# Kernel tuning notes

Measured on AMD Instinct MI355X. Metric: run time of the kernel, lower is better.

Reference implementation:

```python
import jax, jax.numpy as jnp
import numpy as np

B, S, D, UNITS = 32, 2048, 1024, 1024


def setup_inputs() -> dict:
    key = jax.random.key(0)
    ks = jax.random.split(key, 8)
    scale_d = 1.0 / np.sqrt(D)
    scale_u = 1.0 / np.sqrt(UNITS)
    return {
        "query": jax.random.normal(ks[0], (B, D), jnp.float32),
        "values": jax.random.normal(ks[1], (B, S, D), jnp.float32),
        "W1": jax.random.normal(ks[2], (D, UNITS), jnp.float32) * scale_d,
        "b1": jnp.zeros((UNITS,), jnp.float32),
        "W2": jax.random.normal(ks[3], (D, UNITS), jnp.float32) * scale_d,
        "b2": jnp.zeros((UNITS,), jnp.float32),
        "V": jax.random.normal(ks[4], (UNITS, 1), jnp.float32) * scale_u,
        "bV": jnp.zeros((1,), jnp.float32),
    }


def reference(query, values, W1, b1, W2, b2, V, bV):
    # proj of encoder outputs: [B, S, UNITS]
    proj_v = jnp.einsum("bsd,du->bsu", values, W1) + b1
    # proj of query (hidden), broadcast over sequence: [B, 1, UNITS]
    proj_q = (query @ W2 + b2)[:, None, :]
    # scalar score per position: [B, S, 1]
    score = jnp.tanh(proj_v + proj_q) @ V + bV
    # softmax over the sequence axis (axis=1)
    attention_weights = jax.nn.softmax(score, axis=1)  # [B, S, 1]
    # weighted sum of values: [B, D]
    context_vector = jnp.sum(attention_weights * values, axis=1)
    return context_vector, attention_weights
```

## Files before the change

### kernel.cpp

```cpp
#include <hip/hip_runtime.h>
#include <stdint.h>

typedef float f32x4 __attribute__((ext_vector_type(4)));
typedef short bf16x8 __attribute__((ext_vector_type(8)));

#define AS1 __attribute__((address_space(1)))
#define AS3 __attribute__((address_space(3)))

#define NB 32
#define NS 2048
#define ND 1024
#define NU 1024
#define NM (NB * NS)

__device__ __forceinline__ void glds16(const void* g, void* l) {
  __builtin_amdgcn_global_load_lds((const AS1 uint32_t*)g, (AS3 uint32_t*)l, 16, 0, 0);
}

__device__ __forceinline__ unsigned short bf16_rne(float f) {
  uint32_t u = __float_as_uint(f);
  u += 0x7fffu + ((u >> 16) & 1u);
  return (unsigned short)(u >> 16);
}

__device__ __forceinline__ uint32_t pack_bf16_trunc(float lo, float hi) {
  return __builtin_amdgcn_perm(__float_as_uint(hi), __float_as_uint(lo), 0x07060302u);
}

__device__ __forceinline__ float fast_tanh(float x) {
  float e = __expf(2.0f * x);
  return 1.0f - 2.0f / (e + 1.0f);
}

__global__ __launch_bounds__(256) void k_w1t(const float* __restrict__ W1,
                                             unsigned short* __restrict__ W1T) {
  __shared__ float t[64][65];
  const int n0 = blockIdx.x * 64, k0 = blockIdx.y * 64;
  const int tid = threadIdx.x;
  {
    const int r = tid >> 4, c4 = (tid & 15) << 2;
#pragma unroll
    for (int i = 0; i < 4; ++i) {
      f32x4 v = *(const f32x4*)(W1 + (size_t)(k0 + r + i * 16) * NU + n0 + c4);
      t[r + i * 16][c4 + 0] = v.x;
      t[r + i * 16][c4 + 1] = v.y;
      t[r + i * 16][c4 + 2] = v.z;
      t[r + i * 16][c4 + 3] = v.w;
    }
  }
  __syncthreads();
  const int rr = tid >> 2, cc = tid & 3;
  uint32_t o[8];
#pragma unroll
  for (int p = 0; p < 8; ++p) {
    float f0 = t[cc * 16 + 2 * p + 0][rr];
    float f1 = t[cc * 16 + 2 * p + 1][rr];
    o[p] = (uint32_t)bf16_rne(f0) | ((uint32_t)bf16_rne(f1) << 16);
  }
  unsigned short* dst = W1T + (size_t)(n0 + rr) * ND + k0 + cc * 16;
  *(uint4*)(dst + 0) = make_uint4(o[0], o[1], o[2], o[3]);
  *(uint4*)(dst + 8) = make_uint4(o[4], o[5], o[6], o[7]);
}

__global__ __launch_bounds__(256) void k_pq(const float* __restrict__ query,
                                            const float* __restrict__ W2,
                                            const float* __restrict__ b1,
                                            const float* __restrict__ b2,
                                            float* __restrict__ pq) {
  const int u = blockIdx.x * 256 + threadIdx.x;
  const int b = blockIdx.y;
  const float* q = query + b * ND;
  float a0 = b1[u] + b2[u], a1 = 0.f, a2 = 0.f, a3 = 0.f;
  for (int k = 0; k < ND; k += 16) {
#pragma unroll
    for (int j = 0; j < 16; j += 4) {
      a0 = fmaf(q[k + j + 0], W2[(size_t)(k + j + 0) * NU + u], a0);
      a1 = fmaf(q[k + j + 1], W2[(size_t)(k + j + 1) * NU + u], a1);
      a2 = fmaf(q[k + j + 2], W2[(size_t)(k + j + 2) * NU + u], a2);
      a3 = fmaf(q[k + j + 3], W2[(size_t)(k + j + 3) * NU + u], a3);
    }
  }
  pq[b * NU + u] = (a0 + a1) + (a2 + a3);
}

__global__ __launch_bounds__(256) void k_score(const float* __restrict__ values,
                                               const unsigned short* __restrict__ W1T,
                                               const float* __restrict__ pq,
                                               const float* __restrict__ V,
                                               float* __restrict__ score) {
  __shared__ f32x4 lds4[1536];
  char* lds = (char*)lds4;

  const int tid = threadIdx.x;
  const int lane = tid & 63;
  const int w = tid >> 6;
  const int wr = w >> 1, wc = w & 1;
  const int quad = lane >> 4, l15 = lane & 15;

  const int bid = blockIdx.x;
  const int xcd = bid & 7;
  const int local = bid >> 3;
  const int mt = xcd * 64 + (local >> 3);
  const int nc = local & 7;
  const int m0 = mt * 128, n0 = nc * 128;

  const char* aG[4];
  uint32_t aL[4];
  {
    const int p = lane & 7, r3 = lane >> 3;
    const int ca = p ^ r3;
#pragma unroll
    for (int i = 0; i < 4; ++i) {
      const int seg = w * 4 + i;
      const int mloc = seg * 8 + r3;
      aG[i] = (const char*)values + (size_t)(m0 + mloc) * (ND * 4) + ca * 16;
      aL[i] = seg * 1024;
    }
  }
  const char* bG[2];
  uint32_t bL[2];
  {
    const int cb = (lane & 3) ^ ((lane >> 3) & 3);
#pragma unroll
    for (int i = 0; i < 2; ++i) {
      const int seg = w * 2 + i;
      const int nloc = seg * 16 + (lane >> 2);
      bG[i] = (const char*)W1T + (size_t)(n0 + nloc) * (ND * 2) + cb * 16;
      bL[i] = 16384 + seg * 1024;
    }
  }

  uint32_t aOff[4][2], bOff[4];
  {
    const int p0 = (2 * quad) ^ (l15 & 7);
#pragma unroll
    for (int ri = 0; ri < 4; ++ri) {
      const int m = wr * 64 + ri * 16 + l15;
      aOff[ri][0] = m * 128 + p0 * 16;
      aOff[ri][1] = m * 128 + (p0 ^ 1) * 16;
    }
    const int pb = quad ^ ((l15 >> 1) & 3);
#pragma unroll
    for (int ci = 0; ci < 4; ++ci) {
      const int n = wc * 64 + ci * 16 + l15;
      bOff[ci] = 16384 + n * 64 + pb * 16;
    }
  }

  f32x4 acc[4][4];
#pragma unroll
  for (int i = 0; i < 4; ++i)
#pragma unroll
    for (int j = 0; j < 4; ++j) acc[i][j] = (f32x4){0.f, 0.f, 0.f, 0.f};

  for (int kt = 0; kt < 32; ++kt) {
    __syncthreads();
    const size_t aCol = (size_t)kt * 128;
    const size_t bCol = (size_t)kt * 64;
#pragma unroll
    for (int i = 0; i < 4; ++i) glds16(aG[i] + aCol, lds + aL[i]);
#pragma unroll
    for (int i = 0; i < 2; ++i) glds16(bG[i] + bCol, lds + bL[i]);
    __syncthreads();

    bf16x8 af[4];
#pragma unroll
    for (int ri = 0; ri < 4; ++ri) {
      f32x4 v0 = *(const f32x4*)(lds + aOff[ri][0]);
      f32x4 v1 = *(const f32x4*)(lds + aOff[ri][1]);
      union { uint32_t u[4]; bf16x8 v; } cvt;
      cvt.u[0] = pack_bf16_trunc(v0.x, v0.y);
      cvt.u[1] = pack_bf16_trunc(v0.z, v0.w);
      cvt.u[2] = pack_bf16_trunc(v1.x, v1.y);
      cvt.u[3] = pack_bf16_trunc(v1.z, v1.w);
      af[ri] = cvt.v;
    }
    bf16x8 bfg[4];
#pragma unroll
    for (int ci = 0; ci < 4; ++ci) {
      union { f32x4 f; bf16x8 v; } u;
      u.f = *(const f32x4*)(lds + bOff[ci]);
      bfg[ci] = u.v;
    }
#pragma unroll
    for (int ri = 0; ri < 4; ++ri)
#pragma unroll
      for (int ci = 0; ci < 4; ++ci)
        acc[ri][ci] =
            __builtin_amdgcn_mfma_f32_16x16x32_bf16(af[ri], bfg[ci], acc[ri][ci], 0, 0, 0);
  }

  const int b = m0 >> 11;
  float vv[4], qq[4];
#pragma unroll
  for (int ci = 0; ci < 4; ++ci) {
    const int col = n0 + wc * 64 + ci * 16 + l15;
    vv[ci] = V[col];
    qq[ci] = pq[b * NU + col];
  }
#pragma unroll
  for (int ri = 0; ri < 4; ++ri) {
    float p0 = 0.f, p1 = 0.f, p2 = 0.f, p3 = 0.f;
#pragma unroll
    for (int ci = 0; ci < 4; ++ci) {
      f32x4 a = acc[ri][ci];
      p0 += fast_tanh(a.x + qq[ci]) * vv[ci];
      p1 += fast_tanh(a.y + qq[ci]) * vv[ci];
      p2 += fast_tanh(a.z + qq[ci]) * vv[ci];
      p3 += fast_tanh(a.w + qq[ci]) * vv[ci];
    }
#pragma unroll
    for (int mask = 1; mask < 16; mask <<= 1) {
      p0 += __shfl_xor(p0, mask);
      p1 += __shfl_xor(p1, mask);
      p2 += __shfl_xor(p2, mask);
      p3 += __shfl_xor(p3, mask);
    }
    if (l15 == 0) {
      const int rbase = m0 + wr * 64 + ri * 16 + quad * 4;
      atomicAdd(&score[rbase + 0], p0);
      atomicAdd(&score[rbase + 1], p1);
      atomicAdd(&score[rbase + 2], p2);
      atomicAdd(&score[rbase + 3], p3);
    }
  }
}

__global__ __launch_bounds__(256) void k_softmax(const float* __restrict__ score,
                                                 float* __restrict__ attn) {
  __shared__ float red[8];
  const int b = blockIdx.x, tid = threadIdx.x;
  const int w = tid >> 6, lane = tid & 63;
  const float* s = score + b * NS;
  float v[8];
  float mx = -3.4e38f;
#pragma unroll
  for (int j = 0; j < 8; ++j) {
    v[j] = s[tid + j * 256];
    mx = fmaxf(mx, v[j]);
  }
#pragma unroll
  for (int mask = 1; mask < 64; mask <<= 1) mx = fmaxf(mx, __shfl_xor(mx, mask));
  if (lane == 0) red[w] = mx;
  __syncthreads();
  mx = fmaxf(fmaxf(red[0], red[1]), fmaxf(red[2], red[3]));
  float sum = 0.f;
#pragma unroll
  for (int j = 0; j < 8; ++j) {
    v[j] = __expf(v[j] - mx);
    sum += v[j];
  }
#pragma unroll
  for (int mask = 1; mask < 64; mask <<= 1) sum += __shfl_xor(sum, mask);
  if (lane == 0) red[4 + w] = sum;
  __syncthreads();
  const float inv = 1.0f / (red[4] + red[5] + red[6] + red[7]);
  float* o = attn + b * NS;
#pragma unroll
  for (int j = 0; j < 8; ++j) o[tid + j * 256] = v[j] * inv;
}

__global__ __launch_bounds__(256) void k_ctx_part(const float* __restrict__ values,
                                                  const float* __restrict__ attn,
                                                  float* __restrict__ part) {
  const int sc = blockIdx.x, b = blockIdx.y, tid = threadIdx.x;
  const int s0 = sc * 64;
  const f32x4* vb = (const f32x4*)(values + (size_t)(b * NS + s0) * ND);
  const float* ab = attn + b * NS + s0;
  f32x4 acc0 = (f32x4){0.f, 0.f, 0.f, 0.f};
  f32x4 acc1 = (f32x4){0.f, 0.f, 0.f, 0.f};
  for (int s = 0; s < 64; s += 8) {
    f32x4 v0 = vb[(size_t)(s + 0) * 256 + tid];
    f32x4 v1 = vb[(size_t)(s + 1) * 256 + tid];
    f32x4 v2 = vb[(size_t)(s + 2) * 256 + tid];
    f32x4 v3 = vb[(size_t)(s + 3) * 256 + tid];
    f32x4 v4 = vb[(size_t)(s + 4) * 256 + tid];
    f32x4 v5 = vb[(size_t)(s + 5) * 256 + tid];
    f32x4 v6 = vb[(size_t)(s + 6) * 256 + tid];
    f32x4 v7 = vb[(size_t)(s + 7) * 256 + tid];
    acc0 += ab[s + 0] * v0;
    acc1 += ab[s + 1] * v1;
    acc0 += ab[s + 2] * v2;
    acc1 += ab[s + 3] * v3;
    acc0 += ab[s + 4] * v4;
    acc1 += ab[s + 5] * v5;
    acc0 += ab[s + 6] * v6;
    acc1 += ab[s + 7] * v7;
  }
  *(f32x4*)(part + (size_t)(b * 32 + sc) * ND + tid * 4) = acc0 + acc1;
}

__global__ __launch_bounds__(256) void k_ctx_red(const float* __restrict__ part,
                                                 float* __restrict__ ctx) {
  const int b = blockIdx.x, tid = threadIdx.x;
  f32x4 acc = (f32x4){0.f, 0.f, 0.f, 0.f};
#pragma unroll
  for (int sc = 0; sc < 32; ++sc)
    acc += *(const f32x4*)(part + (size_t)(b * 32 + sc) * ND + tid * 4);
  *(f32x4*)(ctx + (size_t)b * ND + tid * 4) = acc;
}

extern "C" void kernel_launch(void* const* d_in, const int* in_sizes, int n_in,
                              void* d_out, int out_size, void* d_ws, size_t ws_size,
                              hipStream_t stream) {
  const float* query  = (const float*)d_in[0];
  const float* values = (const float*)d_in[1];
  const float* W1     = (const float*)d_in[2];
  const float* b1     = (const float*)d_in[3];
  const float* W2     = (const float*)d_in[4];
  const float* b2     = (const float*)d_in[5];
  const float* V      = (const float*)d_in[6];

  char* ws = (char*)d_ws;
  unsigned short* W1T = (unsigned short*)ws;
  float* pq    = (float*)(ws + (2u << 20));
  float* score = (float*)(ws + (2u << 20) + (128u << 10));
  float* part  = (float*)(ws + (2u << 20) + (384u << 10));

  float* ctx  = (float*)d_out;
  float* attn = (float*)d_out + NB * ND;

  hipMemsetAsync(score, 0, NM * sizeof(float), stream);
  k_w1t<<<dim3(16, 16), 256, 0, stream>>>(W1, W1T);
  k_pq<<<dim3(4, NB), 256, 0, stream>>>(query, W2, b1, b2, pq);
  k_score<<<dim3(4096), 256, 0, stream>>>(values, W1T, pq, V, score);
  k_softmax<<<NB, 256, 0, stream>>>(score, attn);
  k_ctx_part<<<dim3(32, NB), 256, 0, stream>>>(values, attn, part);
  k_ctx_red<<<NB, 256, 0, stream>>>(part, ctx);
}
```

Measured before the change: 678.5 us.

## Pre-convert values to fp16 and run score GEMM and context sum in fp16

Result: no change. 665.5 us (-1.9%).

```diff
diff --git a/kernel.cpp b/kernel.cpp
--- a/kernel.cpp
+++ b/kernel.cpp
@@ -3,6 +3,7 @@
 
 typedef float f32x4 __attribute__((ext_vector_type(4)));
 typedef short bf16x8 __attribute__((ext_vector_type(8)));
+typedef _Float16 f16x8 __attribute__((ext_vector_type(8)));
 
 #define AS1 __attribute__((address_space(1)))
 #define AS3 __attribute__((address_space(3)))
@@ -23,6 +24,13 @@
   return (unsigned short)(u >> 16);
 }
 
+__device__ __forceinline__ uint32_t h2pack(float lo, float hi) {
+  union { _Float16 h[2]; uint32_t u; } p;
+  p.h[0] = (_Float16)lo;
+  p.h[1] = (_Float16)hi;
+  return p.u;
+}
+
 __device__ __forceinline__ uint32_t pack_bf16_trunc(float lo, float hi) {
   return __builtin_amdgcn_perm(__float_as_uint(hi), __float_as_uint(lo), 0x07060302u);
 }
@@ -32,8 +40,25 @@
   return 1.0f - 2.0f / (e + 1.0f);
 }
 
-__global__ __launch_bounds__(256) void k_w1t(const float* __restrict__ W1,
-                                             unsigned short* __restrict__ W1T) {
+__global__ __launch_bounds__(256) void k_cvt(const float* __restrict__ values,
+                                             _Float16* __restrict__ values_h) {
+  const size_t gid = (size_t)blockIdx.x * 256 + threadIdx.x;
+#pragma unroll 2
+  for (int it = 0; it < 8; ++it) {
+    const size_t e0 = gid * 8 + (size_t)it * 8388608;
+    f32x4 v0 = *(const f32x4*)(values + e0);
+    f32x4 v1 = *(const f32x4*)(values + e0 + 4);
+    uint4 o;
+    o.x = h2pack(v0.x, v0.y);
+    o.y = h2pack(v0.z, v0.w);
+    o.z = h2pack(v1.x, v1.y);
+    o.w = h2pack(v1.z, v1.w);
+    *(uint4*)(values_h + e0) = o;
+  }
+}
+
+__global__ __launch_bounds__(256) void k_w1t_h(const float* __restrict__ W1,
+                                               _Float16* __restrict__ W1T) {
   __shared__ float t[64][65];
   const int n0 = blockIdx.x * 64, k0 = blockIdx.y * 64;
   const int tid = threadIdx.x;
@@ -52,6 +77,33 @@
   const int rr = tid >> 2, cc = tid & 3;
   uint32_t o[8];
 #pragma unroll
+  for (int p = 0; p < 8; ++p)
+    o[p] = h2pack(t[cc * 16 + 2 * p + 0][rr], t[cc * 16 + 2 * p + 1][rr]);
+  _Float16* dst = W1T + (size_t)(n0 + rr) * ND + k0 + cc * 16;
+  *(uint4*)(dst + 0) = make_uint4(o[0], o[1], o[2], o[3]);
+  *(uint4*)(dst + 8) = make_uint4(o[4], o[5], o[6], o[7]);
+}
+
+__global__ __launch_bounds__(256) void k_w1t(const float* __restrict__ W1,
+                                             unsigned short* __restrict__ W1T) {
+  __shared__ float t[64][65];
+  const int n0 = blockIdx.x * 64, k0 = blockIdx.y * 64;
+  const int tid = threadIdx.x;
+  {
+    const int r = tid >> 4, c4 = (tid & 15) << 2;
+#pragma unroll
+    for (int i = 0; i < 4; ++i) {
+      f32x4 v = *(const f32x4*)(W1 + (size_t)(k0 + r + i * 16) * NU + n0 + c4);
+      t[r + i * 16][c4 + 0] = v.x;
+      t[r + i * 16][c4 + 1] = v.y;
+      t[r + i * 16][c4 + 2] = v.z;
+      t[r + i * 16][c4 + 3] = v.w;
+    }
+  }
+  __syncthreads();
+  const int rr = tid >> 2, cc = tid & 3;
+  uint32_t o[8];
+#pragma unroll
   for (int p = 0; p < 8; ++p) {
     float f0 = t[cc * 16 + 2 * p + 0][rr];
     float f1 = t[cc * 16 + 2 * p + 1][rr];
@@ -64,31 +116,40 @@
 
 __global__ __launch_bounds__(256) void k_pq(const float* __restrict__ query,
                                             const float* __restrict__ W2,
-                                            const float* __restrict__ b1,
-                                            const float* __restrict__ b2,
-                                            float* __restrict__ pq) {
-  const int u = blockIdx.x * 256 + threadIdx.x;
-  const int b = blockIdx.y;
-  const float* q = query + b * ND;
-  float a0 = b1[u] + b2[u], a1 = 0.f, a2 = 0.f, a3 = 0.f;
-  for (int k = 0; k < ND; k += 16) {
-#pragma unroll
-    for (int j = 0; j < 16; j += 4) {
-      a0 = fmaf(q[k + j + 0], W2[(size_t)(k + j + 0) * NU + u], a0);
-      a1 = fmaf(q[k + j + 1], W2[(size_t)(k + j + 1) * NU + u], a1);
-      a2 = fmaf(q[k + j + 2], W2[(size_t)(k + j + 2) * NU + u], a2);
-      a3 = fmaf(q[k + j + 3], W2[(size_t)(k + j + 3) * NU + u], a3);
-    }
-  }
-  pq[b * NU + u] = (a0 + a1) + (a2 + a3);
-}
-
-__global__ __launch_bounds__(256) void k_score(const float* __restrict__ values,
-                                               const unsigned short* __restrict__ W1T,
-                                               const float* __restrict__ pq,
-                                               const float* __restrict__ V,
-                                               float* __restrict__ score) {
-  __shared__ f32x4 lds4[1536];
+                                            float* __restrict__ pq_part) {
+  const int kc = blockIdx.x, b = blockIdx.y;
+  const int u4 = threadIdx.x * 4;
+  const float* q = query + b * ND + kc * 256;
+  f32x4 a0 = (f32x4){0.f, 0.f, 0.f, 0.f}, a1 = a0;
+  const float* w = W2 + (size_t)kc * 256 * NU + u4;
+  for (int k = 0; k < 256; k += 8) {
+#pragma unroll
+    for (int j = 0; j < 8; j += 2) {
+      a0 += q[k + j + 0] * *(const f32x4*)(w + (size_t)(k + j + 0) * NU);
+      a1 += q[k + j + 1] * *(const f32x4*)(w + (size_t)(k + j + 1) * NU);
+    }
+  }
+  *(f32x4*)(pq_part + (size_t)(kc * NB + b) * NU + u4) = a0 + a1;
+}
+
+__global__ __launch_bounds__(256) void k_pq_red(const float* __restrict__ pq_part,
+                                                const float* __restrict__ b1,
+                                                const float* __restrict__ b2,
+                                                float* __restrict__ pq) {
+  const int b = blockIdx.x, u4 = threadIdx.x * 4;
+  f32x4 acc = *(const f32x4*)(b1 + u4) + *(const f32x4*)(b2 + u4);
+#pragma unroll
+  for (int kc = 0; kc < 4; ++kc)
+    acc += *(const f32x4*)(pq_part + (size_t)(kc * NB + b) * NU + u4);
+  *(f32x4*)(pq + (size_t)b * NU + u4) = acc;
+}
+
+__global__ __launch_bounds__(256) void k_score_h(const _Float16* __restrict__ valh,
+                                                 const _Float16* __restrict__ W1T,
+                                                 const float* __restrict__ pq,
+                                                 const float* __restrict__ V,
+                                                 float* __restrict__ score) {
+  __shared__ f32x4 lds4[1024];
   char* lds = (char*)lds4;
 
   const int tid = threadIdx.x;
@@ -104,6 +165,122 @@
   const int nc = local & 7;
   const int m0 = mt * 128, n0 = nc * 128;
 
+  const char* aG[2];
+  const char* bG[2];
+  uint32_t aL[2], bL[2];
+  {
+    const int r = lane >> 2;
+    const int ca = (lane & 3) ^ (r & 3);
+#pragma unroll
+    for (int i = 0; i < 2; ++i) {
+      const int seg = w * 2 + i;
+      const int rloc = seg * 16 + r;
+      aG[i] = (const char*)valh + (size_t)(m0 + rloc) * (ND * 2) + ca * 16;
+      aL[i] = seg * 1024;
+      bG[i] = (const char*)W1T + (size_t)(n0 + rloc) * (ND * 2) + ca * 16;
+      bL[i] = 8192 + seg * 1024;
+    }
+  }
+
+  uint32_t aOff[4], bOff[4];
+  {
+    const int pp = (quad ^ (l15 & 3)) * 16;
+#pragma unroll
+    for (int ri = 0; ri < 4; ++ri) aOff[ri] = (wr * 64 + ri * 16 + l15) * 64 + pp;
+#pragma unroll
+    for (int ci = 0; ci < 4; ++ci) bOff[ci] = 8192 + (wc * 64 + ci * 16 + l15) * 64 + pp;
+  }
+
+  f32x4 acc[4][4];
+#pragma unroll
+  for (int i = 0; i < 4; ++i)
+#pragma unroll
+    for (int j = 0; j < 4; ++j) acc[i][j] = (f32x4){0.f, 0.f, 0.f, 0.f};
+
+  for (int kt = 0; kt < 32; ++kt) {
+    __syncthreads();
+    const size_t col = (size_t)kt * 64;
+#pragma unroll
+    for (int i = 0; i < 2; ++i) glds16(aG[i] + col, lds + aL[i]);
+#pragma unroll
+    for (int i = 0; i < 2; ++i) glds16(bG[i] + col, lds + bL[i]);
+    __syncthreads();
+
+    f16x8 af[4], bf[4];
+#pragma unroll
+    for (int ri = 0; ri < 4; ++ri) {
+      union { f32x4 f; f16x8 h; } u;
+      u.f = *(const f32x4*)(lds + aOff[ri]);
+      af[ri] = u.h;
+    }
+#pragma unroll
+    for (int ci = 0; ci < 4; ++ci) {
+      union { f32x4 f; f16x8 h; } u;
+      u.f = *(const f32x4*)(lds + bOff[ci]);
+      bf[ci] = u.h;
+    }
+#pragma unroll
+    for (int ri = 0; ri < 4; ++ri)
+#pragma unroll
+      for (int ci = 0; ci < 4; ++ci)
+        acc[ri][ci] =
+            __builtin_amdgcn_mfma_f32_16x16x32_f16(af[ri], bf[ci], acc[ri][ci], 0, 0, 0);
+  }
+
+  const int b = m0 >> 11;
+  float vv[4], qq[4];
+#pragma unroll
+  for (int ci = 0; ci < 4; ++ci) {
+    const int col = n0 + wc * 64 + ci * 16 + l15;
+    vv[ci] = V[col];
+    qq[ci] = pq[b * NU + col];
+  }
+#pragma unroll
+  for (int ri = 0; ri < 4; ++ri) {
+    float p0 = 0.f, p1 = 0.f, p2 = 0.f, p3 = 0.f;
+#pragma unroll
+    for (int ci = 0; ci < 4; ++ci) {
+      f32x4 a = acc[ri][ci];
+      p0 += fast_tanh(a.x + qq[ci]) * vv[ci];
+      p1 += fast_tanh(a.y + qq[ci]) * vv[ci];
+      p2 += fast_tanh(a.z + qq[ci]) * vv[ci];
+      p3 += fast_tanh(a.w + qq[ci]) * vv[ci];
+    }
+#pragma unroll
+    for (int mask = 1; mask < 16; mask <<= 1) {
+      p0 += __shfl_xor(p0, mask);
+      p1 += __shfl_xor(p1, mask);
+      p2 += __shfl_xor(p2, mask);
+      p3 += __shfl_xor(p3, mask);
+    }
+    if (l15 == 0) {
+      const int rbase = m0 + wr * 64 + ri * 16 + quad * 4;
+      atomicAdd(&score[rbase + 0], p0);
+      atomicAdd(&score[rbase + 1], p1);
+      atomicAdd(&score[rbase + 2], p2);
+      atomicAdd(&score[rbase + 3], p3);
+    }
+  }
+}
+
+__global__ __launch_bounds__(256) void k_score_f32(const float* __restrict__ values,
+                                                   const unsigned short* __restrict__ W1T,
+                                                   const float* __restrict__ pq,
+                                                   const float* __restrict__ V,
+                                                   float* __restrict__ score) {
+  __shared__ f32x4 lds4[1536];
+  char* lds = (char*)lds4;
+  const int tid = threadIdx.x;
+  const int lane = tid & 63;
+  const int w = tid >> 6;
+  const int wr = w >> 1, wc = w & 1;
+  const int quad = lane >> 4, l15 = lane & 15;
+  const int bid = blockIdx.x;
+  const int xcd = bid & 7;
+  const int local = bid >> 3;
+  const int mt = xcd * 64 + (local >> 3);
+  const int nc = local & 7;
+  const int m0 = mt * 128, n0 = nc * 128;
   const char* aG[4];
   uint32_t aL[4];
   {
@@ -129,7 +306,6 @@
       bL[i] = 16384 + seg * 1024;
     }
   }
-
   uint32_t aOff[4][2], bOff[4];
   {
     const int p0 = (2 * quad) ^ (l15 & 7);
@@ -146,13 +322,11 @@
       bOff[ci] = 16384 + n * 64 + pb * 16;
     }
   }
-
   f32x4 acc[4][4];
 #pragma unroll
   for (int i = 0; i < 4; ++i)
 #pragma unroll
     for (int j = 0; j < 4; ++j) acc[i][j] = (f32x4){0.f, 0.f, 0.f, 0.f};
-
   for (int kt = 0; kt < 32; ++kt) {
     __syncthreads();
     const size_t aCol = (size_t)kt * 128;
@@ -162,7 +336,6 @@
 #pragma unroll
     for (int i = 0; i < 2; ++i) glds16(bG[i] + bCol, lds + bL[i]);
     __syncthreads();
-
     bf16x8 af[4];
 #pragma unroll
     for (int ri = 0; ri < 4; ++ri) {
@@ -189,7 +362,6 @@
         acc[ri][ci] =
             __builtin_amdgcn_mfma_f32_16x16x32_bf16(af[ri], bfg[ci], acc[ri][ci], 0, 0, 0);
   }
-
   const int b = m0 >> 11;
   float vv[4], qq[4];
 #pragma unroll
@@ -260,15 +432,44 @@
   for (int j = 0; j < 8; ++j) o[tid + j * 256] = v[j] * inv;
 }
 
-__global__ __launch_bounds__(256) void k_ctx_part(const float* __restrict__ values,
-                                                  const float* __restrict__ attn,
-                                                  float* __restrict__ part) {
+__global__ __launch_bounds__(128) void k_ctx_part_h(const _Float16* __restrict__ valh,
+                                                    const float* __restrict__ attn,
+                                                    float* __restrict__ part) {
+  const int sc = blockIdx.x, b = blockIdx.y, t = threadIdx.x;
+  const int row0 = b * NS + sc * 32;
+  const int d8 = t * 8;
+  const float* ab = attn + row0;
+  float acc[8];
+#pragma unroll
+  for (int i = 0; i < 8; ++i) acc[i] = 0.f;
+  for (int s0 = 0; s0 < 32; s0 += 8) {
+    uint4 r[8];
+#pragma unroll
+    for (int j = 0; j < 8; ++j)
+      r[j] = *(const uint4*)(valh + (size_t)(row0 + s0 + j) * ND + d8);
+#pragma unroll
+    for (int j = 0; j < 8; ++j) {
+      union { uint4 u; _Float16 h[8]; } c;
+      c.u = r[j];
+      const float a = ab[s0 + j];
+#pragma unroll
+      for (int i = 0; i < 8; ++i) acc[i] = fmaf(a, (float)c.h[i], acc[i]);
+    }
+  }
+  float* o = part + (size_t)(b * 64 + sc) * ND + d8;
+#pragma unroll
+  for (int i = 0; i < 8; ++i) o[i] = acc[i];
+}
+
+__global__ __launch_bounds__(256) void k_ctx_part_f32(const float* __restrict__ values,
+                                                      const float* __restrict__ attn,
+                                                      float* __restrict__ part) {
   const int sc = blockIdx.x, b = blockIdx.y, tid = threadIdx.x;
   const int s0 = sc * 64;
   const f32x4* vb = (const f32x4*)(values + (size_t)(b * NS + s0) * ND);
   const float* ab = attn + b * NS + s0;
   f32x4 acc0 = (f32x4){0.f, 0.f, 0.f, 0.f};
-  f32x4 acc1 = (f32x4){0.f, 0.f, 0.f, 0.f};
+  f32x4 acc1 = acc0;
   for (int s = 0; s < 64; s += 8) {
     f32x4 v0 = vb[(size_t)(s + 0) * 256 + tid];
     f32x4 v1 = vb[(size_t)(s + 1) * 256 + tid];
@@ -291,12 +492,11 @@
 }
 
 __global__ __launch_bounds__(256) void k_ctx_red(const float* __restrict__ part,
-                                                 float* __restrict__ ctx) {
+                                                 float* __restrict__ ctx, int count) {
   const int b = blockIdx.x, tid = threadIdx.x;
   f32x4 acc = (f32x4){0.f, 0.f, 0.f, 0.f};
-#pragma unroll
-  for (int sc = 0; sc < 32; ++sc)
-    acc += *(const f32x4*)(part + (size_t)(b * 32 + sc) * ND + tid * 4);
+  for (int sc = 0; sc < count; ++sc)
+    acc += *(const f32x4*)(part + (size_t)(b * count + sc) * ND + tid * 4);
   *(f32x4*)(ctx + (size_t)b * ND + tid * 4) = acc;
 }
 
@@ -311,20 +511,44 @@
   const float* b2     = (const float*)d_in[5];
   const float* V      = (const float*)d_in[6];
 
-  char* ws = (char*)d_ws;
-  unsigned short* W1T = (unsigned short*)ws;
-  float* pq    = (float*)(ws + (2u << 20));
-  float* score = (float*)(ws + (2u << 20) + (128u << 10));
-  float* part  = (float*)(ws + (2u << 20) + (384u << 10));
-
   float* ctx  = (float*)d_out;
   float* attn = (float*)d_out + NB * ND;
 
-  hipMemsetAsync(score, 0, NM * sizeof(float), stream);
-  k_w1t<<<dim3(16, 16), 256, 0, stream>>>(W1, W1T);
-  k_pq<<<dim3(4, NB), 256, 0, stream>>>(query, W2, b1, b2, pq);
-  k_score<<<dim3(4096), 256, 0, stream>>>(values, W1T, pq, V, score);
-  k_softmax<<<NB, 256, 0, stream>>>(score, attn);
-  k_ctx_part<<<dim3(32, NB), 256, 0, stream>>>(values, attn, part);
-  k_ctx_red<<<NB, 256, 0, stream>>>(part, ctx);
-}
+  char* ws = (char*)d_ws;
+  const size_t SZ_VALH = (size_t)NM * ND * 2;
+  const size_t need_h = SZ_VALH + 2097152 + 524288 + 131072 + 262144 + 8388608;
+
+  if (ws_size >= need_h) {
+    _Float16* valh   = (_Float16*)ws;
+    _Float16* W1Th   = (_Float16*)(ws + SZ_VALH);
+    float* pq_part   = (float*)(ws + SZ_VALH + 2097152);
+    float* pq        = (float*)(ws + SZ_VALH + 2621440);
+    float* score     = (float*)(ws + SZ_VALH + 2752512);
+    float* part      = (float*)(ws + SZ_VALH + 3014656);
+
+    hipMemsetAsync(score, 0, NM * sizeof(float), stream);
+    k_cvt<<<4096, 256, 0, stream>>>(values, valh);
+    k_w1t_h<<<dim3(16, 16), 256, 0, stream>>>(W1, W1Th);
+    k_pq<<<dim3(4, NB), 256, 0, stream>>>(query, W2, pq_part);
+    k_pq_red<<<NB, 256, 0, stream>>>(pq_part, b1, b2, pq);
+    k_score_h<<<4096, 256, 0, stream>>>(valh, W1Th, pq, V, score);
+    k_softmax<<<NB, 256, 0, stream>>>(score, attn);
+    k_ctx_part_h<<<dim3(64, NB), 128, 0, stream>>>(valh, attn, part);
+    k_ctx_red<<<NB, 256, 0, stream>>>(part, ctx, 64);
+  } else {
+    unsigned short* W1T = (unsigned short*)ws;
+    float* pq_part = (float*)(ws + 2097152);
+    float* pq      = (float*)(ws + 2621440);
+    float* score   = (float*)(ws + 2752512);
+    float* part    = (float*)(ws + 3014656);
+
+    hipMemsetAsync(score, 0, NM * sizeof(float), stream);
+    k_w1t<<<dim3(16, 16), 256, 0, stream>>>(W1, W1T);
+    k_pq<<<dim3(4, NB), 256, 0, stream>>>(query, W2, pq_part);
+    k_pq_red<<<NB, 256, 0, stream>>>(pq_part, b1, b2, pq);
+    k_score_f32<<<4096, 256, 0, stream>>>(values, W1T, pq, V, score);
+    k_softmax<<<NB, 256, 0, stream>>>(score, attn);
+    k_ctx_part_f32<<<dim3(32, NB), 256, 0, stream>>>(values, attn, part);
+    k_ctx_red<<<NB, 256, 0, stream>>>(part, ctx, 32);
+  }
+}
```
